# Optimization experiments

Measured on AMD Instinct MI355X. Metric: run time of the kernel, lower is better.

## Reference

```python
import jax, jax.numpy as jnp
import numpy as np

N, E, D, L, NE, FF, G, V, H = 4096, 131072, 256, 4, 2, 512, 128, 100, 8
DK = D // H


def setup_inputs() -> dict:
    key = jax.random.key(0)
    ks = iter(jax.random.split(key, 64))
    def W(shape, scale=0.05):
        return jax.random.normal(next(ks), shape, dtype=jnp.float32) * scale
    inp = {}
    inp['z'] = jax.random.randint(next(ks), (N,), 0, V)
    inp['pos'] = jax.random.normal(next(ks), (N, 3), dtype=jnp.float32)
    inp['batch'] = jnp.sort(jax.random.randint(next(ks), (N,), 0, G))
    inp['edge_index'] = jax.random.randint(next(ks), (2, E), 0, N)
    inp['emb'] = W((V, D))
    # E_GCL stacks (EGNN layer: edge MLP, attention gate, node MLP)
    inp['egcl_edge_w1'] = W((L, 2 * D + 1, D)); inp['egcl_edge_b1'] = jnp.zeros((L, D), jnp.float32)
    inp['egcl_edge_w2'] = W((L, D, D));         inp['egcl_edge_b2'] = jnp.zeros((L, D), jnp.float32)
    inp['egcl_node_w1'] = W((L, 2 * D, D));     inp['egcl_node_b1'] = jnp.zeros((L, D), jnp.float32)
    inp['egcl_node_w2'] = W((L, D, D));         inp['egcl_node_b2'] = jnp.zeros((L, D), jnp.float32)
    inp['egcl_att_w'] = W((L, D, 1));           inp['egcl_att_b'] = jnp.zeros((L, 1), jnp.float32)
    # Transformer encoder stacks (post-norm)
    inp['enc_wq'] = W((NE, D, D)); inp['enc_bq'] = jnp.zeros((NE, D), jnp.float32)
    inp['enc_wk'] = W((NE, D, D)); inp['enc_bk'] = jnp.zeros((NE, D), jnp.float32)
    inp['enc_wv'] = W((NE, D, D)); inp['enc_bv'] = jnp.zeros((NE, D), jnp.float32)
    inp['enc_wo'] = W((NE, D, D)); inp['enc_bo'] = jnp.zeros((NE, D), jnp.float32)
    inp['enc_ln1_g'] = jnp.ones((NE, D), jnp.float32); inp['enc_ln1_b'] = jnp.zeros((NE, D), jnp.float32)
    inp['enc_ffn_w1'] = W((NE, D, FF)); inp['enc_ffn_b1'] = jnp.zeros((NE, FF), jnp.float32)
    inp['enc_ffn_w2'] = W((NE, FF, D)); inp['enc_ffn_b2'] = jnp.zeros((NE, D), jnp.float32)
    inp['enc_ln2_g'] = jnp.ones((NE, D), jnp.float32); inp['enc_ln2_b'] = jnp.zeros((NE, D), jnp.float32)
    # energy_fc head
    inp['fc_w1'] = W((D, D)); inp['fc_b1'] = jnp.zeros((D,), jnp.float32)
    inp['fc_w2'] = W((D, 1)); inp['fc_b2'] = jnp.zeros((1,), jnp.float32)
    return inp


def _layer_norm(x, g, b, eps=1e-5):
    mu = jnp.mean(x, axis=-1, keepdims=True)
    var = jnp.mean((x - mu) ** 2, axis=-1, keepdims=True)
    return (x - mu) * jax.lax.rsqrt(var + eps) * g + b


def reference(z, pos, batch, edge_index, emb,
              egcl_edge_w1, egcl_edge_b1, egcl_edge_w2, egcl_edge_b2,
              egcl_node_w1, egcl_node_b1, egcl_node_w2, egcl_node_b2,
              egcl_att_w, egcl_att_b,
              enc_wq, enc_bq, enc_wk, enc_bk, enc_wv, enc_bv, enc_wo, enc_bo,
              enc_ln1_g, enc_ln1_b, enc_ffn_w1, enc_ffn_b1, enc_ffn_w2, enc_ffn_b2,
              enc_ln2_g, enc_ln2_b, fc_w1, fc_b1, fc_w2, fc_b2):
    h = emb[z]                                   # [N, D]
    row, col = edge_index[0], edge_index[1]
    diff = pos[row] - pos[col]                   # static_coord: coords never updated
    radial = jnp.sum(diff * diff, axis=-1, keepdims=True)  # [E, 1]
    for i in range(L):
        m_in = jnp.concatenate([h[row], h[col], radial], axis=-1)     # [E, 2D+1]
        m = jax.nn.silu(m_in @ egcl_edge_w1[i] + egcl_edge_b1[i])
        m = jax.nn.silu(m @ egcl_edge_w2[i] + egcl_edge_b2[i])        # [E, D]
        m = m * jax.nn.sigmoid(m @ egcl_att_w[i] + egcl_att_b[i])     # attention gate
        agg = jax.ops.segment_sum(m, row, num_segments=N)             # [N, D]
        n_in = jnp.concatenate([h, agg], axis=-1)
        upd = jax.nn.silu(n_in @ egcl_node_w1[i] + egcl_node_b1[i]) @ egcl_node_w2[i] + egcl_node_b2[i]
        h = h + upd                                                   # residual
    scale = 1.0 / jnp.sqrt(jnp.asarray(DK, h.dtype))
    for i in range(NE):
        q = (h @ enc_wq[i] + enc_bq[i]).reshape(N, H, DK)
        k = (h @ enc_wk[i] + enc_bk[i]).reshape(N, H, DK)
        v = (h @ enc_wv[i] + enc_bv[i]).reshape(N, H, DK)
        scores = jnp.einsum('nhd,mhd->hnm', q, k) * scale
        a = jax.nn.softmax(scores, axis=-1)
        attn = jnp.einsum('hnm,mhd->nhd', a, v).reshape(N, D) @ enc_wo[i] + enc_bo[i]
        h = _layer_norm(h + attn, enc_ln1_g[i], enc_ln1_b[i])
        f = jax.nn.silu(h @ enc_ffn_w1[i] + enc_ffn_b1[i]) @ enc_ffn_w2[i] + enc_ffn_b2[i]
        h = _layer_norm(h + f, enc_ln2_g[i], enc_ln2_b[i])
    g = jax.ops.segment_sum(h, batch, num_segments=G)                 # scatter-add readout
    out = jax.nn.silu(g @ fc_w1 + fc_b1) @ fc_w2 + fc_b2              # [G, 1]
    return out
```

## Files before the change

### kernel.cpp

```cpp
#include <hip/hip_runtime.h>
#include <math.h>

#define N_NODES 4096
#define N_EDGES 131072
#define DIM     256
#define NL      4
#define NENC    2
#define FFD     512
#define NG      128
#define NHEAD   8
#define DKH     32
#define TE2     32

typedef __attribute__((ext_vector_type(8))) short bf16x8;
typedef __attribute__((ext_vector_type(4))) float f32x4;

__device__ __forceinline__ float siluf(float x) { return x / (1.f + __expf(-x)); }
__device__ __forceinline__ float sigmf_(float x) { return 1.f / (1.f + __expf(-x)); }
__device__ __forceinline__ unsigned short f2b(float f) {
    union { float f; unsigned u; } x; x.f = f;
    unsigned r = x.u + 0x7fffu + ((x.u >> 16) & 1u);
    return (unsigned short)(r >> 16);
}
__device__ __forceinline__ float b2f(unsigned short h) {
    union { unsigned u; float f; } x; x.u = (unsigned)h << 16; return x.f;
}

__global__ __launch_bounds__(256) void k_embed(const int* __restrict__ z,
                                               const float* __restrict__ emb,
                                               float* __restrict__ h) {
    int i = blockIdx.x * 256 + threadIdx.x;
    int n = i >> 8, d = i & 255;
    h[i] = emb[z[n] * DIM + d];
}

__global__ __launch_bounds__(256) void k_radial(const float* __restrict__ pos,
                                                const int* __restrict__ ei,
                                                float* __restrict__ radial) {
    int e = blockIdx.x * 256 + threadIdx.x;
    if (e >= N_EDGES) return;
    int r = ei[e], c = ei[N_EDGES + e];
    float dx = pos[r*3+0] - pos[c*3+0];
    float dy = pos[r*3+1] - pos[c*3+1];
    float dz = pos[r*3+2] - pos[c*3+2];
    radial[e] = dx*dx + dy*dy + dz*dz;
}

__global__ __launch_bounds__(256) void k_hist(const int* __restrict__ ei, int* __restrict__ cnt) {
    int e = blockIdx.x * 256 + threadIdx.x;
    if (e < N_EDGES) atomicAdd(&cnt[ei[e]], 1);
}

__global__ __launch_bounds__(256) void k_scan(const int* __restrict__ cnt, int* __restrict__ pos) {
    __shared__ int s_w[4];
    int t = threadIdx.x, lane = t & 63, wv = t >> 6;
    int loc[16]; int s = 0;
    #pragma unroll
    for (int i = 0; i < 16; ++i) { loc[i] = s; s += cnt[t * 16 + i]; }
    int inc = s;
    #pragma unroll
    for (int off = 1; off < 64; off <<= 1) {
        int v = __shfl_up(inc, off, 64);
        if (lane >= off) inc += v;
    }
    if (lane == 63) s_w[wv] = inc;
    __syncthreads();
    int wbase = 0;
    for (int j = 0; j < wv; ++j) wbase += s_w[j];
    int base = wbase + inc - s;
    #pragma unroll
    for (int i = 0; i < 16; ++i) pos[t * 16 + i] = base + loc[i];
}

__global__ __launch_bounds__(256) void k_scatter(const int* __restrict__ ei,
                                                 const float* __restrict__ radial,
                                                 int* __restrict__ pos,
                                                 int* __restrict__ rows_s,
                                                 int* __restrict__ cols_s,
                                                 float* __restrict__ rad_s) {
    int e = blockIdx.x * 256 + threadIdx.x;
    if (e >= N_EDGES) return;
    int r = ei[e];
    int p = atomicAdd(&pos[r], 1);
    rows_s[p] = r;
    cols_s[p] = ei[N_EDGES + e];
    rad_s[p] = radial[e];
}

__global__ __launch_bounds__(256) void k_conv_w2(const float* __restrict__ ew2,
                                                 unsigned short* __restrict__ W2F) {
    int tid = blockIdx.x * 256 + threadIdx.x;
    int layer = tid >> 13;
    int r = tid & 8191;
    int ks = r >> 10, ntg = (r >> 6) & 15, lane = r & 63;
    const float* W = ew2 + (size_t)layer * 65536;
    unsigned short tmp[8];
    #pragma unroll
    for (int j = 0; j < 8; ++j) {
        int k = ks*32 + 4*(lane>>4) + (j&3) + 16*(j>>2);
        int n = ntg*16 + (lane&15);
        tmp[j] = f2b(W[k*256 + n]);
    }
    *(bf16x8*)&W2F[(size_t)layer*65536 + (size_t)r*8] = *(const bf16x8*)&tmp[0];
}

__global__ __launch_bounds__(256) void k_pack_all(
    const float* __restrict__ ew1, const float* __restrict__ nw1, const float* __restrict__ nw2,
    const float* __restrict__ wq, const float* __restrict__ wk, const float* __restrict__ wv,
    const float* __restrict__ wo, const float* __restrict__ fw1, const float* __restrict__ fw2,
    unsigned short* __restrict__ dst)
{
    int f = blockIdx.x * 256 + threadIdx.x;
    int rem, panel, NTG, mode;
    if (f < 65536)       { rem = f;          panel = rem / 16384; rem &= 16383; NTG = 32; mode = 0; }
    else if (f < 131072) { rem = f - 65536;  panel = rem / 16384; rem &= 16383; NTG = 16; mode = 1; }
    else if (f < 163840) { rem = f - 131072; panel = rem / 8192;  rem &= 8191;  NTG = 16; mode = 2; }
    else if (f < 212992) { rem = f - 163840; panel = rem / 24576; rem %= 24576; NTG = 48; mode = 3; }
    else if (f < 229376) { rem = f - 212992; panel = rem / 8192;  rem &= 8191;  NTG = 16; mode = 4; }
    else if (f < 262144) { rem = f - 229376; panel = rem / 16384; rem &= 16383; NTG = 32; mode = 5; }
    else                 { rem = f - 262144; panel = rem / 16384; rem &= 16383; NTG = 16; mode = 6; }
    int ks   = rem / (NTG * 64);
    int ntg  = (rem >> 6) % NTG;
    int lane = rem & 63;
    unsigned short tmp[8];
    #pragma unroll
    for (int j = 0; j < 8; ++j) {
        int k = ks*32 + 4*(lane>>4) + (j&3) + 16*(j>>2);
        int n = ntg*16 + (lane&15);
        float val;
        switch (mode) {
            case 0: val = ew1[(size_t)panel*131328 + (n < 256 ? k*256 + n : (256 + k)*256 + (n - 256))]; break;
            case 1: val = nw1[(size_t)panel*131072 + k*256 + n]; break;
            case 2: val = nw2[(size_t)panel*65536 + k*256 + n]; break;
            case 3: { const float* b = (n < 256) ? wq : ((n < 512) ? wk : wv);
                      val = b[(size_t)panel*65536 + k*256 + (n & 255)]; } break;
            case 4: val = wo[(size_t)panel*65536 + k*256 + n]; break;
            case 5: val = fw1[(size_t)panel*131072 + k*512 + n]; break;
            default: val = fw2[(size_t)panel*131072 + k*256 + n]; break;
        }
        tmp[j] = f2b(val);
    }
    *(bf16x8*)&dst[(size_t)f * 8] = *(const bf16x8*)&tmp[0];
}

template<int NCHUNK, int NC, int NSPLIT, int ACT, int RESID, int OUTMODE>
__global__ __launch_bounds__(256) void k_gemm(
    const float* __restrict__ A0, const float* __restrict__ A1, int lda,
    const unsigned short* __restrict__ Wp,
    const float* __restrict__ b0, const float* __restrict__ b1, const float* __restrict__ b2,
    const float* __restrict__ resid, float* __restrict__ C,
    unsigned short* __restrict__ kpk, unsigned short* __restrict__ vpk)
{
    constexpr int NT  = NC / (64 * NSPLIT);
    constexpr int NTG = NC / 16;
    __shared__ __align__(16) char s_hi[16 * 512];
    __shared__ __align__(16) char s_lo[16 * 512];
    const int t = threadIdx.x, l = t & 63, w = t >> 6;
    const int g = l >> 4, r = l & 15;
    const int mtile  = blockIdx.x % 256;
    const int nchunk = blockIdx.x / 256;
    const int r0 = mtile * 16;

    f32x4 acc[NT];
    #pragma unroll
    for (int nt = 0; nt < NT; ++nt) acc[nt] = (f32x4){0.f, 0.f, 0.f, 0.f};

    const bf16x8* Wf = (const bf16x8*)Wp;
    for (int c = 0; c < NCHUNK; ++c) {
        const float* Ac = (c == 0) ? A0 : A1;
        __syncthreads();
        const int c4 = l * 4;
        #pragma unroll
        for (int it = 0; it < 4; ++it) {
            int row = it * 4 + w;
            float4 v = *(const float4*)&Ac[(size_t)(r0 + row) * lda + c4];
            float vv[4] = {v.x, v.y, v.z, v.w};
            ushort4 h4, l4;
            unsigned short hh;
            hh = f2b(vv[0]); h4.x = hh; l4.x = f2b(vv[0] - b2f(hh));
            hh = f2b(vv[1]); h4.y = hh; l4.y = f2b(vv[1] - b2f(hh));
            hh = f2b(vv[2]); h4.z = hh; l4.z = f2b(vv[2] - b2f(hh));
            hh = f2b(vv[3]); h4.w = hh; l4.w = f2b(vv[3] - b2f(hh));
            int boff = (c4 * 2) ^ (row << 3);
            *(ushort4*)&s_hi[row * 512 + boff] = h4;
            *(ushort4*)&s_lo[row * 512 + boff] = l4;
        }
        __syncthreads();
        #pragma unroll
        for (int ks = 0; ks < 8; ++ks) {
            const int ksg = c * 8 + ks;
            const int x0 = (ks * 64 + 8 * g) ^ (r << 3);
            union { uint2 u[2]; bf16x8 v; } ah, al;
            ah.u[0] = *(const uint2*)&s_hi[r * 512 + x0];
            ah.u[1] = *(const uint2*)&s_hi[r * 512 + (x0 ^ 32)];
            al.u[0] = *(const uint2*)&s_lo[r * 512 + x0];
            al.u[1] = *(const uint2*)&s_lo[r * 512 + (x0 ^ 32)];
            #pragma unroll
            for (int nt = 0; nt < NT; ++nt) {
                int fb = (nchunk * 4 + w) * NT + nt;
                bf16x8 bf_ = Wf[(size_t)(ksg * NTG + fb) * 64 + l];
                acc[nt] = __builtin_amdgcn_mfma_f32_16x16x32_bf16(ah.v, bf_, acc[nt], 0, 0, 0);
                acc[nt] = __builtin_amdgcn_mfma_f32_16x16x32_bf16(al.v, bf_, acc[nt], 0, 0, 0);
            }
        }
    }
    #pragma unroll
    for (int nt = 0; nt < NT; ++nt) {
        int n = ((nchunk * 4 + w) * NT + nt) * 16 + r;
        float bias = 0.f;
        if (b0) {
            const float* bp = (n < 256) ? b0 : ((n < 512) ? b1 : b2);
            bias = bp[n & 255];
        }
        #pragma unroll
        for (int reg = 0; reg < 4; ++reg) {
            int row = r0 + g * 4 + reg;
            float v = acc[nt][reg] + bias;
            if (ACT == 1) v = siluf(v);
            if (RESID) v += resid[(size_t)row * 256 + n];
            if (OUTMODE == 0) {
                C[(size_t)row * NC + n] = v;
            } else {
                if (n < 256) {
                    C[(size_t)row * 256 + n] = v;
                } else if (n < 512) {
                    int hd = (n - 256) >> 5, dm = (n - 256) & 31;
                    int dp = (dm & 3) | (((dm >> 4) & 1) << 2) | (((dm >> 2) & 3) << 3);
                    unsigned short hb = f2b(v);
                    size_t base = ((size_t)hd * N_NODES + row) * 64;
                    kpk[base + dp]      = hb;
                    kpk[base + 32 + dp] = f2b(v - b2f(hb));
                } else {
                    int hd = (n - 512) >> 5, dm = (n - 512) & 31;
                    int s = row & 31;
                    int sp = (s & 3) | (((s >> 4) & 1) << 2) | (((s >> 2) & 3) << 3);
                    int keyp = (row & ~31) | sp;
                    vpk[((size_t)hd * 32 + dm) * N_NODES + keyp] = f2b(v);
                }
            }
        }
    }
}

__global__ __launch_bounds__(256) void k_edge_mfma(
    const float* __restrict__ P12,
    const int* __restrict__ rows_s, const int* __restrict__ cols_s,
    const float* __restrict__ rad_s,
    const float* __restrict__ w1r, const float* __restrict__ b1,
    const unsigned short* __restrict__ W2F, const float* __restrict__ b2,
    const float* __restrict__ aw, const float* __restrict__ ab,
    float* __restrict__ agg)
{
    __shared__ __align__(16) char s_a[TE2 * 512];
    __shared__ int   s_row[TE2], s_cn[TE2];
    __shared__ float s_rad[TE2], s_gp[4][TE2], s_gate[TE2];
    const int t = threadIdx.x, l = t & 63, w = t >> 6;
    const int e0 = blockIdx.x * TE2;

    if (t < TE2) {
        s_row[t] = rows_s[e0 + t];
        s_cn[t]  = cols_s[e0 + t];
        s_rad[t] = rad_s[e0 + t];
    }
    __syncthreads();

    const int c4 = l * 4;
    const float4 wr = *(const float4*)&w1r[c4];
    const float4 bb = *(const float4*)&b1[c4];
    #pragma unroll
    for (int it = 0; it < 8; ++it) {
        int e = it * 4 + w;
        float4 pa = *(const float4*)&P12[(size_t)s_row[e] * 512 + c4];
        float4 pb = *(const float4*)&P12[(size_t)s_cn[e] * 512 + 256 + c4];
        float rad = s_rad[e];
        ushort4 pk;
        pk.x = f2b(siluf(pa.x + pb.x + rad * wr.x + bb.x));
        pk.y = f2b(siluf(pa.y + pb.y + rad * wr.y + bb.y));
        pk.z = f2b(siluf(pa.z + pb.z + rad * wr.z + bb.z));
        pk.w = f2b(siluf(pa.w + pb.w + rad * wr.w + bb.w));
        *(ushort4*)&s_a[e * 512 + ((c4 * 2) ^ ((e & 15) << 3))] = pk;
    }
    __syncthreads();

    const int g = l >> 4, r = l & 15;
    f32x4 acc[2][4];
    #pragma unroll
    for (int mt = 0; mt < 2; ++mt)
        #pragma unroll
        for (int nt = 0; nt < 4; ++nt)
            acc[mt][nt] = (f32x4){0.f, 0.f, 0.f, 0.f};

    const bf16x8* Wf = (const bf16x8*)W2F;
    for (int ks = 0; ks < 8; ++ks) {
        bf16x8 af[2], bfr[4];
        #pragma unroll
        for (int mt = 0; mt < 2; ++mt) {
            int rowa = mt * 16 + r;
            int x0 = (ks * 64 + 8 * g) ^ (r << 3);
            uint2 lo = *(const uint2*)&s_a[rowa * 512 + x0];
            uint2 hi = *(const uint2*)&s_a[rowa * 512 + (x0 ^ 32)];
            union { uint2 u[2]; bf16x8 v; } ua;
            ua.u[0] = lo; ua.u[1] = hi;
            af[mt] = ua.v;
        }
        #pragma unroll
        for (int nt = 0; nt < 4; ++nt)
            bfr[nt] = Wf[(ks * 16 + w * 4 + nt) * 64 + l];
        #pragma unroll
        for (int mt = 0; mt < 2; ++mt)
            #pragma unroll
            for (int nt = 0; nt < 4; ++nt)
                acc[mt][nt] = __builtin_amdgcn_mfma_f32_16x16x32_bf16(af[mt], bfr[nt], acc[mt][nt], 0, 0, 0);
    }

    float b2v[4], awv[4];
    #pragma unroll
    for (int nt = 0; nt < 4; ++nt) {
        int col = w * 64 + nt * 16 + r;
        b2v[nt] = b2[col];
        awv[nt] = aw[col];
    }
    float pg[2][4];
    #pragma unroll
    for (int mt = 0; mt < 2; ++mt)
        #pragma unroll
        for (int reg = 0; reg < 4; ++reg) {
            float s = 0.f;
            #pragma unroll
            for (int nt = 0; nt < 4; ++nt) {
                float v = siluf(acc[mt][nt][reg] + b2v[nt]);
                acc[mt][nt][reg] = v;
                s += v * awv[nt];
            }
            pg[mt][reg] = s;
        }
    #pragma unroll
    for (int off = 1; off < 16; off <<= 1)
        #pragma unroll
        for (int mt = 0; mt < 2; ++mt)
            #pragma unroll
            for (int reg = 0; reg < 4; ++reg)
                pg[mt][reg] += __shfl_xor(pg[mt][reg], off, 64);
    if (r == 0) {
        #pragma unroll
        for (int mt = 0; mt < 2; ++mt)
            #pragma unroll
            for (int reg = 0; reg < 4; ++reg)
                s_gp[w][mt * 16 + g * 4 + reg] = pg[mt][reg];
    }
    __syncthreads();
    if (t < TE2)
        s_gate[t] = sigmf_(s_gp[0][t] + s_gp[1][t] + s_gp[2][t] + s_gp[3][t] + ab[0]);
    __syncthreads();

    unsigned short* s_out = (unsigned short*)s_a;
    #pragma unroll
    for (int mt = 0; mt < 2; ++mt)
        #pragma unroll
        for (int reg = 0; reg < 4; ++reg) {
            int el = mt * 16 + g * 4 + reg;
            float gt = s_gate[el];
            #pragma unroll
            for (int nt = 0; nt < 4; ++nt)
                s_out[el * 256 + w * 64 + nt * 16 + r] = f2b(acc[mt][nt][reg] * gt);
        }
    __syncthreads();
    float cur = 0.f;
    for (int e = 0; e < TE2; ++e) {
        cur += b2f(s_out[e * 256 + t]);
        bool flush = (e == TE2 - 1) || (s_row[e + 1] != s_row[e]);
        if (flush) {
            atomicAdd(&agg[(size_t)s_row[e] * DIM + t], cur);
            cur = 0.f;
        }
    }
}

template<int ACT>
__global__ __launch_bounds__(256) void k_mlp_small(
    const float* __restrict__ A1, const float* __restrict__ W,
    const float* __restrict__ bias, float* __restrict__ C)
{
    __shared__ float s_a[16][260];
    const int t  = threadIdx.x;
    const int r0 = blockIdx.x * 16;
    for (int r = 0; r < 16; ++r)
        s_a[r][t] = A1[(size_t)(r0 + r) * DIM + t];
    __syncthreads();
    const int er0 = (t >> 6) * 4;
    const int c0 = (t & 63) * 4;
    float acc[4][4];
    #pragma unroll
    for (int e = 0; e < 4; ++e)
        #pragma unroll
        for (int c = 0; c < 4; ++c) acc[e][c] = 0.f;
    #pragma unroll 2
    for (int k = 0; k < DIM; k += 4) {
        float4 w0 = *(const float4*)&W[(size_t)(k+0)*DIM + c0];
        float4 w1 = *(const float4*)&W[(size_t)(k+1)*DIM + c0];
        float4 w2 = *(const float4*)&W[(size_t)(k+2)*DIM + c0];
        float4 w3 = *(const float4*)&W[(size_t)(k+3)*DIM + c0];
        #pragma unroll
        for (int e = 0; e < 4; ++e) {
            float4 x = *(const float4*)&s_a[er0+e][k];
            acc[e][0] += x.x*w0.x + x.y*w1.x + x.z*w2.x + x.w*w3.x;
            acc[e][1] += x.x*w0.y + x.y*w1.y + x.z*w2.y + x.w*w3.y;
            acc[e][2] += x.x*w0.z + x.y*w1.z + x.z*w2.z + x.w*w3.z;
            acc[e][3] += x.x*w0.w + x.y*w1.w + x.z*w2.w + x.w*w3.w;
        }
    }
    float4 bb = *(const float4*)&bias[c0];
    #pragma unroll
    for (int e = 0; e < 4; ++e) {
        float v0 = acc[e][0] + bb.x, v1 = acc[e][1] + bb.y;
        float v2 = acc[e][2] + bb.z, v3 = acc[e][3] + bb.w;
        if (ACT == 1) { v0 = siluf(v0); v1 = siluf(v1); v2 = siluf(v2); v3 = siluf(v3); }
        float4 o; o.x = v0; o.y = v1; o.z = v2; o.w = v3;
        *(float4*)&C[(size_t)(r0 + er0 + e) * DIM + c0] = o;
    }
}

__global__ __launch_bounds__(256) void k_ln(const float* __restrict__ x,
                                            const float* __restrict__ g,
                                            const float* __restrict__ b,
                                            float* __restrict__ out) {
    int t = threadIdx.x, lane = t & 63, w = t >> 6;
    int row = blockIdx.x * 4 + w;
    float4 v = *(const float4*)&x[(size_t)row * DIM + lane * 4];
    float s = v.x + v.y + v.z + v.w;
    #pragma unroll
    for (int off = 32; off; off >>= 1) s += __shfl_xor(s, off, 64);
    float mu = s * (1.f / 256.f);
    float dx = v.x - mu, dy = v.y - mu, dz = v.z - mu, dw = v.w - mu;
    float q = dx*dx + dy*dy + dz*dz + dw*dw;
    #pragma unroll
    for (int off = 32; off; off >>= 1) q += __shfl_xor(q, off, 64);
    float rs = rsqrtf(q * (1.f / 256.f) + 1e-5f);
    float4 gg = *(const float4*)&g[lane * 4];
    float4 bb = *(const float4*)&b[lane * 4];
    float4 o;
    o.x = dx * rs * gg.x + bb.x;
    o.y = dy * rs * gg.y + bb.y;
    o.z = dz * rs * gg.z + bb.z;
    o.w = dw * rs * gg.w + bb.w;
    *(float4*)&out[(size_t)row * DIM + lane * 4] = o;
}

__global__ __launch_bounds__(256) void k_attn_mfma(
    const float* __restrict__ q,
    const unsigned short* __restrict__ kpk,
    const unsigned short* __restrict__ vpk,
    float* __restrict__ o)
{
    __shared__ __align__(16) char s_k[2][8192];
    __shared__ __align__(16) char s_v[2][4096];
    const int t = threadIdx.x, lane = t & 63, w = t >> 6;
    const int g = lane >> 4, r = lane & 15;
    const int head = blockIdx.y;
    const int q0 = blockIdx.x * 64;
    const float scale = 0.17677669529663687f;

    bf16x8 qh, ql;
    {
        const float* qp = &q[(size_t)(q0 + w*16 + r) * DIM + head*DKH + 4*g];
        float4 f0 = *(const float4*)qp;
        float4 f1 = *(const float4*)(qp + 16);
        float vv[8] = {f0.x, f0.y, f0.z, f0.w, f1.x, f1.y, f1.z, f1.w};
        union { unsigned short s[8]; bf16x8 v; } uh, ul;
        #pragma unroll
        for (int j = 0; j < 8; ++j) {
            float sv = vv[j] * scale;
            unsigned short hb = f2b(sv);
            uh.s[j] = hb;
            ul.s[j] = f2b(sv - b2f(hb));
        }
        qh = uh.v; ql = ul.v;
    }

    const char* kbase = (const char*)(kpk + (size_t)head * N_NODES * 64);
    const unsigned short* vbase = vpk + (size_t)head * 32 * N_NODES;
    const int vrow = t >> 3, vch = t & 7;

    uint4 kr0, kr1, vr0;
    {
        const char* kt = kbase;
        kr0 = *(const uint4*)(kt + t * 16);
        kr1 = *(const uint4*)(kt + 4096 + t * 16);
        vr0 = *(const uint4*)(vbase + (size_t)vrow * N_NODES + vch * 8);
        int key0 = t >> 3, sl0 = t & 7;
        *(uint4*)&s_k[0][key0 * 128 + ((sl0 ^ (key0 & 7)) << 4)] = kr0;
        int c1 = t + 256, key1 = c1 >> 3, sl1 = c1 & 7;
        *(uint4*)&s_k[0][key1 * 128 + ((sl1 ^ (key1 & 7)) << 4)] = kr1;
        *(uint4*)&s_v[0][vrow * 128 + ((vch ^ (vrow & 7)) << 4)] = vr0;
    }
    __syncthreads();

    float m = -1e30f, l = 0.f;
    f32x4 ot0 = (f32x4){0.f,0.f,0.f,0.f}, ot1 = (f32x4){0.f,0.f,0.f,0.f};

    for (int tile = 0; tile < 64; ++tile) {
        const int cur = tile & 1;
        if (tile < 63) {
            const char* kt = kbase + (size_t)(tile + 1) * 8192;
            kr0 = *(const uint4*)(kt + t * 16);
            kr1 = *(const uint4*)(kt + 4096 + t * 16);
            vr0 = *(const uint4*)(vbase + (size_t)vrow * N_NODES + (tile + 1) * 64 + vch * 8);
        }
        bf16x8 kh[4], kl[4];
        #pragma unroll
        for (int kb = 0; kb < 4; ++kb) {
            int key = kb * 16 + r;
            kh[kb] = *(const bf16x8*)&s_k[cur][key * 128 + ((g ^ (r & 7)) << 4)];
            kl[kb] = *(const bf16x8*)&s_k[cur][key * 128 + (((4 + g) ^ (r & 7)) << 4)];
        }
        f32x4 sc[4];
        #pragma unroll
        for (int kb = 0; kb < 4; ++kb) {
            f32x4 a = (f32x4){0.f,0.f,0.f,0.f};
            a = __builtin_amdgcn_mfma_f32_16x16x32_bf16(kh[kb], qh, a, 0, 0, 0);
            a = __builtin_amdgcn_mfma_f32_16x16x32_bf16(kh[kb], ql, a, 0, 0, 0);
            a = __builtin_amdgcn_mfma_f32_16x16x32_bf16(kl[kb], qh, a, 0, 0, 0);
            sc[kb] = a;
        }
        float tm = -1e30f;
        #pragma unroll
        for (int kb = 0; kb < 4; ++kb)
            #pragma unroll
            for (int e = 0; e < 4; ++e) tm = fmaxf(tm, sc[kb][e]);
        tm = fmaxf(tm, __shfl_xor(tm, 16, 64));
        tm = fmaxf(tm, __shfl_xor(tm, 32, 64));
        float nm = fmaxf(m, tm);
        float scf = __expf(m - nm);
        m = nm;
        float p[16]; float ls = 0.f;
        #pragma unroll
        for (int kb = 0; kb < 4; ++kb)
            #pragma unroll
            for (int e = 0; e < 4; ++e) {
                float pe = __expf(sc[kb][e] - nm);
                p[kb*4+e] = pe; ls += pe;
            }
        ls += __shfl_xor(ls, 16, 64);
        ls += __shfl_xor(ls, 32, 64);
        l = l * scf + ls;
        ot0[0] *= scf; ot0[1] *= scf; ot0[2] *= scf; ot0[3] *= scf;
        ot1[0] *= scf; ot1[1] *= scf; ot1[2] *= scf; ot1[3] *= scf;
        union { unsigned short s[8]; bf16x8 v; } pk0, pk1;
        #pragma unroll
        for (int j = 0; j < 8; ++j) {
            pk0.s[j] = f2b(p[(j >> 2) * 4 + (j & 3)]);
            pk1.s[j] = f2b(p[(2 + (j >> 2)) * 4 + (j & 3)]);
        }
        bf16x8 vf00 = *(const bf16x8*)&s_v[cur][(0*16 + r) * 128 + (((0*4 + g) ^ (r & 7)) << 4)];
        bf16x8 vf01 = *(const bf16x8*)&s_v[cur][(0*16 + r) * 128 + (((1*4 + g) ^ (r & 7)) << 4)];
        bf16x8 vf10 = *(const bf16x8*)&s_v[cur][(1*16 + r) * 128 + (((0*4 + g) ^ (r & 7)) << 4)];
        bf16x8 vf11 = *(const bf16x8*)&s_v[cur][(1*16 + r) * 128 + (((1*4 + g) ^ (r & 7)) << 4)];
        ot0 = __builtin_amdgcn_mfma_f32_16x16x32_bf16(vf00, pk0.v, ot0, 0, 0, 0);
        ot0 = __builtin_amdgcn_mfma_f32_16x16x32_bf16(vf01, pk1.v, ot0, 0, 0, 0);
        ot1 = __builtin_amdgcn_mfma_f32_16x16x32_bf16(vf10, pk0.v, ot1, 0, 0, 0);
        ot1 = __builtin_amdgcn_mfma_f32_16x16x32_bf16(vf11, pk1.v, ot1, 0, 0, 0);

        __syncthreads();
        if (tile < 63) {
            int key0 = t >> 3, sl0 = t & 7;
            *(uint4*)&s_k[cur ^ 1][key0 * 128 + ((sl0 ^ (key0 & 7)) << 4)] = kr0;
            int c1 = t + 256, key1 = c1 >> 3, sl1 = c1 & 7;
            *(uint4*)&s_k[cur ^ 1][key1 * 128 + ((sl1 ^ (key1 & 7)) << 4)] = kr1;
            *(uint4*)&s_v[cur ^ 1][vrow * 128 + ((vch ^ (vrow & 7)) << 4)] = vr0;
        }
        __syncthreads();
    }

    float inv = 1.f / l;
    float* op = &o[(size_t)(q0 + w*16 + r) * DIM + head*DKH];
    *(float4*)(op + 4*g)      = make_float4(ot0[0]*inv, ot0[1]*inv, ot0[2]*inv, ot0[3]*inv);
    *(float4*)(op + 16 + 4*g) = make_float4(ot1[0]*inv, ot1[1]*inv, ot1[2]*inv, ot1[3]*inv);
}

__global__ __launch_bounds__(256) void k_segsum(const float* __restrict__ h,
                                                const int* __restrict__ batch,
                                                float* __restrict__ gbuf) {
    int i = blockIdx.x * 256 + threadIdx.x;
    int n = i >> 8, d = i & 255;
    atomicAdd(&gbuf[batch[n] * DIM + d], h[i]);
}

__global__ __launch_bounds__(256) void k_head2(const float* __restrict__ gmid,
                                               const float* __restrict__ w2,
                                               const float* __restrict__ b2,
                                               float* __restrict__ out) {
    int t = threadIdx.x, lane = t & 63, w = t >> 6;
    int g = blockIdx.x * 4 + w;
    float4 x  = *(const float4*)&gmid[g * DIM + lane * 4];
    float4 ww = *(const float4*)&w2[lane * 4];
    float s = x.x * ww.x + x.y * ww.y + x.z * ww.z + x.w * ww.w;
    #pragma unroll
    for (int off = 32; off; off >>= 1) s += __shfl_xor(s, off, 64);
    if (lane == 0) out[g] = s + b2[0];
}

extern "C" void kernel_launch(void* const* d_in, const int* in_sizes, int n_in,
                              void* d_out, int out_size, void* d_ws, size_t ws_size,
                              hipStream_t stream)
{
    const int*   z     = (const int*)d_in[0];
    const float* pos   = (const float*)d_in[1];
    const int*   batch = (const int*)d_in[2];
    const int*   ei    = (const int*)d_in[3];
    const float* emb   = (const float*)d_in[4];
    const float* ew1   = (const float*)d_in[5];
    const float* eb1   = (const float*)d_in[6];
    const float* ew2   = (const float*)d_in[7];
    const float* eb2   = (const float*)d_in[8];
    const float* nw1   = (const float*)d_in[9];
    const float* nb1   = (const float*)d_in[10];
    const float* nw2   = (const float*)d_in[11];
    const float* nb2   = (const float*)d_in[12];
    const float* aw    = (const float*)d_in[13];
    const float* ab    = (const float*)d_in[14];
    const float* wq    = (const float*)d_in[15];
    const float* bq    = (const float*)d_in[16];
    const float* wk    = (const float*)d_in[17];
    const float* bk    = (const float*)d_in[18];
    const float* wv    = (const float*)d_in[19];
    const float* bv    = (const float*)d_in[20];
    const float* wo    = (const float*)d_in[21];
    const float* bo    = (const float*)d_in[22];
    const float* ln1g  = (const float*)d_in[23];
    const float* ln1b  = (const float*)d_in[24];
    const float* fw1   = (const float*)d_in[25];
    const float* fb1   = (const float*)d_in[26];
    const float* fw2   = (const float*)d_in[27];
    const float* fb2   = (const float*)d_in[28];
    const float* ln2g  = (const float*)d_in[29];
    const float* ln2b  = (const float*)d_in[30];
    const float* fcw1  = (const float*)d_in[31];
    const float* fcb1  = (const float*)d_in[32];
    const float* fcw2  = (const float*)d_in[33];
    const float* fcb2  = (const float*)d_in[34];
    float* out = (float*)d_out;

    float* ws = (float*)d_ws;
    const size_t ND = (size_t)N_NODES * DIM;
    float* h    = ws;
    float* agg  = ws + ND;
    float* A    = ws + 2 * ND;
    float* U    = ws + 3 * ND;
    float* Bffn = ws + 6 * ND;
    unsigned short* kpk = (unsigned short*)Bffn;
    unsigned short* vpk = kpk + (size_t)NHEAD * N_NODES * 64;
    float* radial = Bffn + (3 * ND) / 2;
    int*   cnt    = (int*)(radial + N_EDGES);
    int*   pcur   = cnt + N_NODES;
    float* gbuf   = ws + 8 * ND;
    float* gmid   = gbuf + (size_t)NG * DIM;
    float* rad_s  = gmid + (size_t)NG * DIM;
    int*   rows_s = (int*)(rad_s + N_EDGES);
    int*   cols_s = rows_s + N_EDGES;
    unsigned short* W2F   = (unsigned short*)(cols_s + N_EDGES);
    unsigned short* packs = W2F + (size_t)NL * 65536;

    unsigned short* PK_W1   = packs;
    unsigned short* PK_NW1  = packs + 524288;
    unsigned short* PK_NW2  = packs + 1048576;
    unsigned short* PK_QKV  = packs + 1310720;
    unsigned short* PK_WO   = packs + 1703936;
    unsigned short* PK_FFN1 = packs + 1835008;
    unsigned short* PK_FFN2 = packs + 2097152;

    dim3 b256(256);

    k_embed<<<N_NODES * DIM / 256, b256, 0, stream>>>(z, emb, h);
    k_radial<<<N_EDGES / 256, b256, 0, stream>>>(pos, ei, radial);
    k_conv_w2<<<NL * 8192 / 256, b256, 0, stream>>>(ew2, W2F);
    k_pack_all<<<1152, b256, 0, stream>>>(ew1, nw1, nw2, wq, wk, wv, wo, fw1, fw2, packs);

    hipMemsetAsync(cnt, 0, N_NODES * sizeof(int), stream);
    k_hist<<<N_EDGES / 256, b256, 0, stream>>>(ei, cnt);
    k_scan<<<1, b256, 0, stream>>>(cnt, pcur);
    k_scatter<<<N_EDGES / 256, b256, 0, stream>>>(ei, radial, pcur, rows_s, cols_s, rad_s);

    for (int l = 0; l < NL; ++l) {
        hipMemsetAsync(agg, 0, ND * sizeof(float), stream);
        const float* W1l = ew1 + (size_t)l * 513 * DIM;
        k_gemm<1,512,2,0,0,0><<<512, b256, 0, stream>>>(h, nullptr, DIM,
            PK_W1 + (size_t)l * 131072, nullptr, nullptr, nullptr, nullptr, U,
            nullptr, nullptr);
        k_edge_mfma<<<N_EDGES / TE2, b256, 0, stream>>>(U, rows_s, cols_s, rad_s,
            W1l + (size_t)512 * DIM, eb1 + (size_t)l * DIM,
            W2F + (size_t)l * 65536, eb2 + (size_t)l * DIM,
            aw + (size_t)l * DIM, ab + l, agg);
        const float* nb1l = nb1 + (size_t)l * DIM;
        k_gemm<2,256,2,1,0,0><<<512, b256, 0, stream>>>(h, agg, DIM,
            PK_NW1 + (size_t)l * 131072, nb1l, nb1l, nb1l, nullptr, A,
            nullptr, nullptr);
        const float* nb2l = nb2 + (size_t)l * DIM;
        k_gemm<1,256,2,0,1,0><<<512, b256, 0, stream>>>(A, nullptr, DIM,
            PK_NW2 + (size_t)l * 65536, nb2l, nb2l, nb2l, h, h,
            nullptr, nullptr);
    }

    for (int i = 0; i < NENC; ++i) {
        k_gemm<1,768,3,0,0,1><<<768, b256, 0, stream>>>(h, nullptr, DIM,
            PK_QKV + (size_t)i * 196608,
            bq + (size_t)i * DIM, bk + (size_t)i * DIM, bv + (size_t)i * DIM, nullptr, U,
            kpk, vpk);
        dim3 ag(N_NODES / 64, NHEAD);
        k_attn_mfma<<<ag, b256, 0, stream>>>(U, kpk, vpk, A);
        const float* bol = bo + (size_t)i * DIM;
        k_gemm<1,256,2,0,1,0><<<512, b256, 0, stream>>>(A, nullptr, DIM,
            PK_WO + (size_t)i * 65536, bol, bol, bol, h, agg,
            nullptr, nullptr);
        k_ln<<<N_NODES / 4, b256, 0, stream>>>(agg, ln1g + (size_t)i * DIM, ln1b + (size_t)i * DIM, h);
        const float* fb1l = fb1 + (size_t)i * FFD;
        k_gemm<1,512,2,1,0,0><<<512, b256, 0, stream>>>(h, nullptr, DIM,
            PK_FFN1 + (size_t)i * 131072, fb1l, fb1l + 256, nullptr, nullptr, Bffn,
            nullptr, nullptr);
        const float* fb2l = fb2 + (size_t)i * DIM;
        k_gemm<2,256,2,0,1,0><<<512, b256, 0, stream>>>(Bffn, Bffn + 256, FFD,
            PK_FFN2 + (size_t)i * 131072, fb2l, fb2l, fb2l, h, agg,
            nullptr, nullptr);
        k_ln<<<N_NODES / 4, b256, 0, stream>>>(agg, ln2g + (size_t)i * DIM, ln2b + (size_t)i * DIM, h);
    }

    hipMemsetAsync(gbuf, 0, (size_t)NG * DIM * sizeof(float), stream);
    k_segsum<<<N_NODES * DIM / 256, b256, 0, stream>>>(h, batch, gbuf);
    k_mlp_small<1><<<NG / 16, b256, 0, stream>>>(gbuf, fcw1, fcb1, gmid);
    k_head2<<<NG / 4, b256, 0, stream>>>(gmid, fcw2, fcb2, out);
}
```

Before: 676.3 us.

## Store edge projections in bf16, transpose edge output tile, streamline attention softmax

The per-layer node projection GEMM now writes bf16 instead of fp32, which halves the bytes that the edge kernel gathers per edge. The edge kernel's output staging is transposed with padding so each thread reads its column with vector loads during the segmented reduction. Separately, the attention kernel folds log2(e) into the scale and uses exp2f, rescales the running accumulators only when some lane's row maximum grows, and packs probabilities with a hardware bf16 pack instruction. These edits trade some precision (bf16 projections) for less memory traffic and fewer ALU operations.

Measured after the change: 679.4 us. About the same (+0.5%).

```diff
diff --git a/kernel.cpp b/kernel.cpp
--- a/kernel.cpp
+++ b/kernel.cpp
@@ -24,6 +24,11 @@
 }
 __device__ __forceinline__ float b2f(unsigned short h) {
     union { unsigned u; float f; } x; x.u = (unsigned)h << 16; return x.f;
+}
+__device__ __forceinline__ unsigned cvtpk(float lo, float hi) {
+    unsigned r;
+    asm("v_cvt_pk_bf16_f32 %0, %1, %2" : "=v"(r) : "v"(lo), "v"(hi));
+    return r;
 }
 
 __global__ __launch_bounds__(256) void k_embed(const int* __restrict__ z,
@@ -220,6 +225,8 @@
             if (RESID) v += resid[(size_t)row * 256 + n];
             if (OUTMODE == 0) {
                 C[(size_t)row * NC + n] = v;
+            } else if (OUTMODE == 2) {
+                ((unsigned short*)C)[(size_t)row * NC + n] = f2b(v);
             } else {
                 if (n < 256) {
                     C[(size_t)row * 256 + n] = v;
@@ -243,7 +250,7 @@
 }
 
 __global__ __launch_bounds__(256) void k_edge_mfma(
-    const float* __restrict__ P12,
+    const unsigned short* __restrict__ P12,
     const int* __restrict__ rows_s, const int* __restrict__ cols_s,
     const float* __restrict__ rad_s,
     const float* __restrict__ w1r, const float* __restrict__ b1,
@@ -251,7 +258,7 @@
     const float* __restrict__ aw, const float* __restrict__ ab,
     float* __restrict__ agg)
 {
-    __shared__ __align__(16) char s_a[TE2 * 512];
+    __shared__ __align__(16) char s_a[20480];
     __shared__ int   s_row[TE2], s_cn[TE2];
     __shared__ float s_rad[TE2], s_gp[4][TE2], s_gate[TE2];
     const int t = threadIdx.x, l = t & 63, w = t >> 6;
@@ -270,14 +277,14 @@
     #pragma unroll
     for (int it = 0; it < 8; ++it) {
         int e = it * 4 + w;
-        float4 pa = *(const float4*)&P12[(size_t)s_row[e] * 512 + c4];
-        float4 pb = *(const float4*)&P12[(size_t)s_cn[e] * 512 + 256 + c4];
+        ushort4 pa4 = *(const ushort4*)&P12[(size_t)s_row[e] * 512 + c4];
+        ushort4 pb4 = *(const ushort4*)&P12[(size_t)s_cn[e] * 512 + 256 + c4];
         float rad = s_rad[e];
         ushort4 pk;
-        pk.x = f2b(siluf(pa.x + pb.x + rad * wr.x + bb.x));
-        pk.y = f2b(siluf(pa.y + pb.y + rad * wr.y + bb.y));
-        pk.z = f2b(siluf(pa.z + pb.z + rad * wr.z + bb.z));
-        pk.w = f2b(siluf(pa.w + pb.w + rad * wr.w + bb.w));
+        pk.x = f2b(siluf(b2f(pa4.x) + b2f(pb4.x) + rad * wr.x + bb.x));
+        pk.y = f2b(siluf(b2f(pa4.y) + b2f(pb4.y) + rad * wr.y + bb.y));
+        pk.z = f2b(siluf(b2f(pa4.z) + b2f(pb4.z) + rad * wr.z + bb.z));
+        pk.w = f2b(siluf(b2f(pa4.w) + b2f(pb4.w) + rad * wr.w + bb.w));
         *(ushort4*)&s_a[e * 512 + ((c4 * 2) ^ ((e & 15) << 3))] = pk;
     }
     __syncthreads();
@@ -355,23 +362,34 @@
 
     unsigned short* s_out = (unsigned short*)s_a;
     #pragma unroll
-    for (int mt = 0; mt < 2; ++mt)
-        #pragma unroll
-        for (int reg = 0; reg < 4; ++reg) {
-            int el = mt * 16 + g * 4 + reg;
-            float gt = s_gate[el];
-            #pragma unroll
-            for (int nt = 0; nt < 4; ++nt)
-                s_out[el * 256 + w * 64 + nt * 16 + r] = f2b(acc[mt][nt][reg] * gt);
-        }
+    for (int mt = 0; mt < 2; ++mt) {
+        float4 gt4 = *(const float4*)&s_gate[mt * 16 + g * 4];
+        #pragma unroll
+        for (int nt = 0; nt < 4; ++nt) {
+            int col = w * 64 + nt * 16 + r;
+            ushort4 o4;
+            o4.x = f2b(acc[mt][nt][0] * gt4.x);
+            o4.y = f2b(acc[mt][nt][1] * gt4.y);
+            o4.z = f2b(acc[mt][nt][2] * gt4.z);
+            o4.w = f2b(acc[mt][nt][3] * gt4.w);
+            *(ushort4*)&s_out[col * 40 + mt * 16 + g * 4] = o4;
+        }
+    }
     __syncthreads();
     float cur = 0.f;
-    for (int e = 0; e < TE2; ++e) {
-        cur += b2f(s_out[e * 256 + t]);
-        bool flush = (e == TE2 - 1) || (s_row[e + 1] != s_row[e]);
-        if (flush) {
-            atomicAdd(&agg[(size_t)s_row[e] * DIM + t], cur);
-            cur = 0.f;
+    #pragma unroll
+    for (int c = 0; c < 4; ++c) {
+        union { uint4 q; unsigned short s[8]; } ch;
+        ch.q = *(const uint4*)&s_out[t * 40 + c * 8];
+        #pragma unroll
+        for (int j = 0; j < 8; ++j) {
+            int e = c * 8 + j;
+            cur += b2f(ch.s[j]);
+            bool flush = (e == TE2 - 1) || (s_row[e + 1] != s_row[e]);
+            if (flush) {
+                atomicAdd(&agg[(size_t)s_row[e] * DIM + t], cur);
+                cur = 0.f;
+            }
         }
     }
 }
@@ -458,7 +476,7 @@
     const int g = lane >> 4, r = lane & 15;
     const int head = blockIdx.y;
     const int q0 = blockIdx.x * 64;
-    const float scale = 0.17677669529663687f;
+    const float scale = 0.17677669529663687f * 1.4426950408889634f;
 
     bf16x8 qh, ql;
     {
@@ -530,27 +548,30 @@
         tm = fmaxf(tm, __shfl_xor(tm, 16, 64));
         tm = fmaxf(tm, __shfl_xor(tm, 32, 64));
         float nm = fmaxf(m, tm);
-        float scf = __expf(m - nm);
-        m = nm;
+        bool grow = tm > m;
+        if (__any(grow)) {
+            float scf = exp2f(m - nm);
+            l *= scf;
+            ot0[0] *= scf; ot0[1] *= scf; ot0[2] *= scf; ot0[3] *= scf;
+            ot1[0] *= scf; ot1[1] *= scf; ot1[2] *= scf; ot1[3] *= scf;
+            m = nm;
+        }
         float p[16]; float ls = 0.f;
         #pragma unroll
         for (int kb = 0; kb < 4; ++kb)
             #pragma unroll
             for (int e = 0; e < 4; ++e) {
-                float pe = __expf(sc[kb][e] - nm);
+                float pe = exp2f(sc[kb][e] - m);
                 p[kb*4+e] = pe; ls += pe;
             }
         ls += __shfl_xor(ls, 16, 64);
         ls += __shfl_xor(ls, 32, 64);
-        l = l * scf + ls;
-        ot0[0] *= scf; ot0[1] *= scf; ot0[2] *= scf; ot0[3] *= scf;
-        ot1[0] *= scf; ot1[1] *= scf; ot1[2] *= scf; ot1[3] *= scf;
-        union { unsigned short s[8]; bf16x8 v; } pk0, pk1;
-        #pragma unroll
-        for (int j = 0; j < 8; ++j) {
-            pk0.s[j] = f2b(p[(j >> 2) * 4 + (j & 3)]);
-            pk1.s[j] = f2b(p[(2 + (j >> 2)) * 4 + (j & 3)]);
-        }
+        l += ls;
+        union { unsigned u[4]; bf16x8 v; } pk0, pk1;
+        pk0.u[0] = cvtpk(p[0], p[1]);  pk0.u[1] = cvtpk(p[2], p[3]);
+        pk0.u[2] = cvtpk(p[4], p[5]);  pk0.u[3] = cvtpk(p[6], p[7]);
+        pk1.u[0] = cvtpk(p[8], p[9]);  pk1.u[1] = cvtpk(p[10], p[11]);
+        pk1.u[2] = cvtpk(p[12], p[13]); pk1.u[3] = cvtpk(p[14], p[15]);
         bf16x8 vf00 = *(const bf16x8*)&s_v[cur][(0*16 + r) * 128 + (((0*4 + g) ^ (r & 7)) << 4)];
         bf16x8 vf01 = *(const bf16x8*)&s_v[cur][(0*16 + r) * 128 + (((1*4 + g) ^ (r & 7)) << 4)];
         bf16x8 vf10 = *(const bf16x8*)&s_v[cur][(1*16 + r) * 128 + (((0*4 + g) ^ (r & 7)) << 4)];
@@ -683,10 +704,11 @@
     for (int l = 0; l < NL; ++l) {
         hipMemsetAsync(agg, 0, ND * sizeof(float), stream);
         const float* W1l = ew1 + (size_t)l * 513 * DIM;
-        k_gemm<1,512,2,0,0,0><<<512, b256, 0, stream>>>(h, nullptr, DIM,
+        k_gemm<1,512,2,0,0,2><<<512, b256, 0, stream>>>(h, nullptr, DIM,
             PK_W1 + (size_t)l * 131072, nullptr, nullptr, nullptr, nullptr, U,
             nullptr, nullptr);
-        k_edge_mfma<<<N_EDGES / TE2, b256, 0, stream>>>(U, rows_s, cols_s, rad_s,
+        k_edge_mfma<<<N_EDGES / TE2, b256, 0, stream>>>((const unsigned short*)U,
+            rows_s, cols_s, rad_s,
             W1l + (size_t)512 * DIM, eb1 + (size_t)l * DIM,
             W2F + (size_t)l * 65536, eb2 + (size_t)l * DIM,
             aw + (size_t)l * DIM, ab + l, agg);
```
